# Kernel optimization log

Hardware: AMD Instinct MI355X
Metric: run time of the kernel (lower is better)

The kernel has to match this reference:

```python
import jax, jax.numpy as jnp
import numpy as np

BS, N, HD = 16, 96, 128      # batch, nodes per graph, hidden_nf
NL, NS = 4, 2                # n_layers, inv_sublayers
ND, HF = 3, 6                # n_dims, node feature dims (in_node_nf - time)
FIN = HF + 1                 # +1 time channel (condition_time=True)
NF = 100.0                   # normalization_factor, aggregation='sum'


def setup_inputs() -> dict:
    key = jax.random.key(0)
    ks = iter(jax.random.split(key, 40))

    def w(shape, scale=None):
        s = scale if scale is not None else 1.0 / np.sqrt(shape[-2])
        return jax.random.normal(next(ks), shape, jnp.float32) * s

    xh = jax.random.normal(next(ks), (BS, N, ND + HF), jnp.float32)
    t = jnp.array([0.5], jnp.float32)
    nm = (jax.random.uniform(next(ks), (BS, N, 1)) < 0.9).astype(jnp.float32)
    em = nm[:, :, None, :] * nm[:, None, :, :]
    em = em * (1.0 - jnp.eye(N, dtype=jnp.float32)[None, :, :, None])
    G = NL * NS
    return dict(
        xh=xh, t=t, node_mask=nm, edge_mask=em,
        W_emb=w((FIN, HD)), b_emb=jnp.zeros((HD,), jnp.float32),
        gWe1=w((G, 2 * HD + 2, HD)), gbe1=jnp.zeros((G, HD), jnp.float32),
        gWe2=w((G, HD, HD)), gbe2=jnp.zeros((G, HD), jnp.float32),
        gWn1=w((G, 2 * HD, HD)), gbn1=jnp.zeros((G, HD), jnp.float32),
        gWn2=w((G, HD, HD)), gbn2=jnp.zeros((G, HD), jnp.float32),
        eWc1=w((NL, 2 * HD + 2, HD)), ebc1=jnp.zeros((NL, HD), jnp.float32),
        eWc2=w((NL, HD, HD)), ebc2=jnp.zeros((NL, HD), jnp.float32),
        eWc3=w((NL, HD, 1), scale=0.001),   # xavier gain 0.001 as in EDM
        W_out=w((HD, FIN)), b_out=jnp.zeros((FIN,), jnp.float32),
    )


def _pair_mlp(h, ea, W1, b1, W2, b2):
    # silu(Linear(cat([h_i, h_j, ea]))) -> silu(Linear) without materializing the concat
    hi = h @ W1[:HD]            # (B,N,H) source part
    hj = h @ W1[HD:2 * HD]      # (B,N,H) target part
    m = jax.nn.silu(hi[:, :, None, :] + hj[:, None, :, :] + ea @ W1[2 * HD:] + b1)
    return jax.nn.silu(m @ W2 + b2)          # (B,N,N,H)


def _egnn(xh, t, node_mask, edge_mask, W_emb, b_emb, gWe1, gbe1, gWe2, gbe2,
          gWn1, gbn1, gWn2, gbn2, eWc1, ebc1, eWc2, ebc2, eWc3, W_out, b_out):
    xh = xh * node_mask                       # mask padded nodes
    x0 = xh[..., :ND]                         # (B,N,3)
    h_time = jnp.broadcast_to(t.reshape(1, 1, 1), (xh.shape[0], xh.shape[1], 1))
    h = jnp.concatenate([xh[..., ND:], h_time], axis=-1)   # (B,N,FIN)
    h = h @ W_emb + b_emb                     # node embedding
    # initial squared distances (EGNN-level edge_attr, in_edge_nf=1)
    d0 = jnp.sum((x0[:, :, None] - x0[:, None, :]) ** 2, -1, keepdims=True)
    x = x0
    for l in range(NL):                       # EquivariantBlocks
        diff = x[:, :, None] - x[:, None, :]  # x_i - x_j, (B,N,N,3)
        radial = jnp.sum(diff ** 2, -1, keepdims=True)
        coord_diff = diff / jnp.sqrt(radial + 1e-8)   # norm_constant=0
        ea = jnp.concatenate([radial, d0], axis=-1)   # (B,N,N,2)
        for s in range(NS):                   # GCL sublayers
            g = l * NS + s
            m = _pair_mlp(h, ea, gWe1[g], gbe1[g], gWe2[g], gbe2[g]) * edge_mask
            agg = jnp.sum(m, axis=2) / NF     # masked scatter-sum over j onto i
            u = jax.nn.silu(h @ gWn1[g, :HD] + agg @ gWn1[g, HD:] + gbn1[g])
            h = (h + (u @ gWn2[g] + gbn2[g])) * node_mask
        # EquivariantUpdate (tanh=False)
        phi = _pair_mlp(h, ea, eWc1[l], ebc1[l], eWc2[l], ebc2[l])
        trans = coord_diff * (phi @ eWc3[l]) * edge_mask    # (B,N,N,3)
        x = (x + jnp.sum(trans, axis=2) / NF) * node_mask
    h = (h @ W_out + b_out) * node_mask       # embedding_out
    vel = (x - x0) * node_mask
    # remove_mean_with_mask
    n_per = jnp.sum(node_mask, axis=1, keepdims=True)
    vel = vel - (jnp.sum(vel, axis=1, keepdims=True) / n_per) * node_mask
    # drop the appended time channel from h (condition_time=True, context=None)
    return jnp.concatenate([vel, h[..., :HF]], axis=-1)    # (B,N,3+HF)


def reference(xh, t, node_mask, edge_mask, W_emb, b_emb, gWe1, gbe1, gWe2, gbe2,
              gWn1, gbn1, gWn2, gbn2, eWc1, ebc1, eWc2, ebc2, eWc3, W_out, b_out):
    return _egnn(xh, t, node_mask, edge_mask, W_emb, b_emb, gWe1, gbe1, gWe2, gbe2,
                 gWn1, gbn1, gWn2, gbn2, eWc1, ebc1, eWc2, ebc2, eWc3, W_out, b_out)
```

## Files before the change

### kernel.cpp

```cpp
#include <hip/hip_runtime.h>
#include <hip/hip_bf16.h>

#define BSZ 16
#define Nn 96
#define HD 128
#define NDIM 3
#define HFEAT 6
#define FINC 7
#define BN (BSZ*Nn)

typedef const float* fp;
typedef __bf16 bf16x8_t __attribute__((ext_vector_type(8)));
typedef float  f32x4_t  __attribute__((ext_vector_type(4)));

__device__ __forceinline__ float silu(float x){ return x / (1.f + __expf(-x)); }
__device__ __forceinline__ unsigned short f2b(float x){
  unsigned u = __float_as_uint(x);
  unsigned r = u + 0x7FFF + ((u>>16)&1);
  return (unsigned short)(r>>16);
}
__device__ __forceinline__ unsigned pkf(float a, float b){
  __hip_bfloat162 h2 = __float22bfloat162_rn(make_float2(a,b));
  return *reinterpret_cast<unsigned*>(&h2);
}


__global__ void k_prep(fp gWe1, fp eWc1, fp gWe2, fp eWc2, fp gWn1, fp gWn2,
                       unsigned short* w1b, unsigned short* w2b,
                       unsigned short* wn1b, unsigned short* wn2b){
  int mid = blockIdx.x;
  if (mid < 12){
    const float* src = (mid<8)? gWe1 + (size_t)mid*258*HD : eWc1 + (size_t)(mid-8)*258*HD;
    unsigned short* dst = w1b + (size_t)mid*32768;
    for (int idx = threadIdx.x; idx < 32768; idx += 256){
      int jj = idx&7, l=(idx>>3)&63, kt=(idx>>9)&3, nt=idx>>11;
      int k = kt*32 + (l>>4)*8 + jj, n = nt*16 + (l&15);
      dst[idx] = f2b(src[(size_t)(k + ((n>>7)<<7))*HD + (n&127)]);
    }
  } else if (mid < 24){
    int m2 = mid-12;
    const float* src = (m2<8)? gWe2 + (size_t)m2*HD*HD : eWc2 + (size_t)(m2-8)*HD*HD;
    unsigned short* dst = w2b + (size_t)m2*HD*HD;
    for (int idx = threadIdx.x; idx < HD*HD; idx += 256){
      int jj = idx&7, l=(idx>>3)&63, kt=(idx>>9)&3, nt=idx>>11;
      int k = kt*32 + (l>>4)*8 + jj, n = nt*16 + (l&15);
      dst[idx] = f2b(src[k*HD+n]);
    }
  } else if (mid < 32){
    int g = mid-24;
    const float* src = gWn1 + (size_t)g*256*HD;
    unsigned short* dst = wn1b + (size_t)g*32768;
    for (int idx = threadIdx.x; idx < 32768; idx += 256){
      int jj = idx&7, l=(idx>>3)&63, kt=(idx>>9)&7, nt=idx>>12;
      int k = kt*32 + (l>>4)*8 + jj, n = nt*16 + (l&15);
      dst[idx] = f2b(src[(size_t)k*HD+n]);
    }
  } else {
    int g = mid-32;
    const float* src = gWn2 + (size_t)g*HD*HD;
    unsigned short* dst = wn2b + (size_t)g*HD*HD;
    for (int idx = threadIdx.x; idx < HD*HD; idx += 256){
      int jj = idx&7, l=(idx>>3)&63, kt=(idx>>9)&3, nt=idx>>11;
      int k = kt*32 + (l>>4)*8 + jj, n = nt*16 + (l&15);
      dst[idx] = f2b(src[k*HD+n]);
    }
  }
}

__global__ void k_embed(fp xh, fp t, fp nm, fp W_emb, fp b_emb,
                        float* h, float* x0, float* xA){
  int bn = blockIdx.x, tid = threadIdx.x;
  float nmv = nm[bn];
  if (tid < NDIM){
    float v = xh[bn*(NDIM+HFEAT)+tid] * nmv;
    x0[bn*3+tid] = v; xA[bn*3+tid] = v;
  }
  float acc = b_emb[tid];
  #pragma unroll
  for (int f=0; f<HFEAT; ++f)
    acc += xh[bn*(NDIM+HFEAT)+NDIM+f] * nmv * W_emb[f*HD+tid];
  acc += t[0] * W_emb[HFEAT*HD+tid];
  h[bn*HD+tid] = acc;
}

__global__ __launch_bounds__(256) void k_hij(const float* hin, const unsigned short* w1m,
                                             fp b1, float* Hi, float* Hj){
  __shared__ unsigned int hf[4*256];
  int tid=threadIdx.x, blk=blockIdx.x;
  int b = blk/6, mt = blk%6;
  int l=tid&63, w=tid>>6;
  { int kp=l, jsub=w;
    int kt=kp>>4, q=(kp>>2)&3, dsub=kp&3;
    int sm = kt + 4*(q&1);
    float2 hv[4];
    #pragma unroll
    for(int r=0;r<4;++r)
      hv[r] = ((const float2*)&hin[(size_t)(b*Nn+mt*16+jsub*4+r)*HD])[kp];
    #pragma unroll
    for(int r=0;r<4;++r){
      int row=jsub*4+r;
      hf[kt*256 + (((row + 16*q) ^ sm)<<2) + dsub] = pkf(hv[r].x,hv[r].y);
    } }
  __syncthreads();
  f32x4_t acc[4];
  #pragma unroll
  for(int s=0;s<4;++s) acc[s]=(f32x4_t){0.f,0.f,0.f,0.f};
  #pragma unroll
  for(int kt=0;kt<4;++kt){
    int pl = l ^ (kt + 4*((l>>4)&1));
    bf16x8_t A = *(const bf16x8_t*)((const unsigned int*)hf + kt*256 + pl*4);
    #pragma unroll
    for(int s=0;s<4;++s){
      bf16x8_t B = *(const bf16x8_t*)(w1m + ((((w*4+s)*4+kt)*64 + l)*8));
      acc[s]=__builtin_amdgcn_mfma_f32_16x16x32_bf16(A, B, acc[s], 0,0,0);
    }
  }
  #pragma unroll
  for(int s=0;s<4;++s){
    int nt=w*4+s, n=nt*16+(l&15);
    float b1v = (nt<8)? b1[n] : 0.f;
    #pragma unroll
    for(int r=0;r<4;++r){
      int R = b*Nn + mt*16 + (l>>4)*4 + r;
      float v = acc[s][r];
      if(nt<8) Hi[(size_t)R*HD+n] = v + b1v;
      else     Hj[(size_t)R*HD+(n-128)] = v;
    }
  }
}

__global__ __launch_bounds__(256,4) void k_pair(const float* Hi, const float* Hj,
    const float* x, const float* x0, fp nm, fp W1f,
    const unsigned short* w2m, fp b2, float* agg){
  __shared__ unsigned int m1f[24*256];
  __shared__ float xs[Nn][3], x0s[Nn][3], nms[Nn], rs[Nn], d0s[Nn];
  __shared__ float red[2][HD];
  int tid=threadIdx.x, bn=blockIdx.x;
  int b=bn/Nn, i=bn%Nn;
  int l=tid&63, w=tid>>6, wm=w>>1, wn=w&1;
  int jg=w;

  for(int idx=tid; idx<Nn*3; idx+=256){ int n=idx/3,d=idx%3;
    xs[n][d]=x[(b*Nn+n)*3+d]; x0s[n][d]=x0[(b*Nn+n)*3+d]; }
  if(tid<Nn) nms[tid]=nm[b*Nn+tid];
  __syncthreads();
  if(tid<Nn){
    float dx0=xs[i][0]-xs[tid][0], dx1=xs[i][1]-xs[tid][1], dx2=xs[i][2]-xs[tid][2];
    rs[tid]=dx0*dx0+dx1*dx1+dx2*dx2;
    float e0=x0s[i][0]-x0s[tid][0], e1=x0s[i][1]-x0s[tid][1], e2=x0s[i][2]-x0s[tid][2];
    d0s[tid]=e0*e0+e1*e1+e2*e2;
  }
  __syncthreads();

  { int kp=l;
    int kt2=kp>>4, q=(kp>>2)&3, dsub=kp&3;
    int sm=kt2+4*(q&1);
    float2 hi=((const float2*)&Hi[(size_t)bn*HD])[kp];
    float2 wr=((const float2*)&W1f[(size_t)(2*HD)*HD])[kp];
    float2 wd=((const float2*)&W1f[(size_t)(2*HD+1)*HD])[kp];
    const float2* HjB=(const float2*)&Hj[(size_t)(b*Nn)*HD];
    #pragma unroll
    for(int half=0; half<2; ++half){
      float2 hjv[12];
      #pragma unroll
      for(int u=0;u<12;++u){
        int rr=half*2+(u/6), mt2=u%6;
        int j=mt2*16+jg*4+rr;
        hjv[u]=HjB[(size_t)j*64+kp];
      }
      #pragma unroll
      for(int u=0;u<12;++u){
        int rr=half*2+(u/6), mt2=u%6;
        int jr=jg*4+rr, j=mt2*16+jr;
        float rv=rs[j], dv=d0s[j];
        float m0 =silu(hi.x+hjv[u].x+rv*wr.x+dv*wd.x);
        float m1v=silu(hi.y+hjv[u].y+rv*wr.y+dv*wd.y);
        m1f[mt2*1024 + kt2*256 + (((jr+16*q)^sm)<<2) + dsub]=pkf(m0,m1v);
      }
    } }
  __syncthreads();

  f32x4_t acc[3][4];
  #pragma unroll
  for(int a=0;a<3;++a)
    #pragma unroll
    for(int s=0;s<4;++s) acc[a][s]=(f32x4_t){0.f,0.f,0.f,0.f};
  #pragma unroll
  for(int kt=0;kt<4;++kt){
    int pl = l ^ (kt + 4*((l>>4)&1));
    bf16x8_t Bk[4];
    #pragma unroll
    for(int s=0;s<4;++s)
      Bk[s] = *(const bf16x8_t*)(w2m + ((((wn*4+s)*4+kt)*64 + l)*8));
    #pragma unroll
    for(int a=0;a<3;++a){
      bf16x8_t A = *(const bf16x8_t*)((const unsigned int*)m1f + (((wm*3+a)*4+kt)*256 + pl*4));
      #pragma unroll
      for(int s=0;s<4;++s)
        acc[a][s]=__builtin_amdgcn_mfma_f32_16x16x32_bf16(A, Bk[s], acc[a][s], 0,0,0);
    }
  }

  float b2v[4], p[4]={0.f,0.f,0.f,0.f};
  #pragma unroll
  for(int s=0;s<4;++s) b2v[s]=b2[(wn*4+s)*16 + (l&15)];
  #pragma unroll
  for(int a=0;a<3;++a)
    #pragma unroll
    for(int r=0;r<4;++r){
      int j=(wm*3+a)*16 + (l>>4)*4 + r;
      float emj=(j==i)?0.f:nms[j];
      #pragma unroll
      for(int s=0;s<4;++s) p[s] += silu(acc[a][s][r]+b2v[s])*emj;
    }
  #pragma unroll
  for(int s=0;s<4;++s){ p[s]+=__shfl_xor(p[s],16); p[s]+=__shfl_xor(p[s],32); }
  if(l<16){
    #pragma unroll
    for(int s=0;s<4;++s) red[wm][wn*64 + s*16 + l]=p[s];
  }
  __syncthreads();
  if(tid<HD) agg[(size_t)bn*HD+tid]=(red[0][tid]+red[1][tid])*nms[i]*(1.f/100.f);
}

__global__ __launch_bounds__(256) void k_nodehij(
    const float* hin, float* hout, const float* agg, fp nm,
    const unsigned short* wn1m, fp bn1v, const unsigned short* wn2m, fp bn2v,
    const unsigned short* w1mA, fp b1A, float* HiA, float* HjA,
    const unsigned short* w1mB, fp b1B, float* HiB, float* HjB){
  __shared__ unsigned int af[8*256];
  __shared__ float fbuf[16*132];
  __shared__ float nmr[16];
  int tid=threadIdx.x, blk=blockIdx.x;
  int b=blk/6, mt=blk%6;
  int R0=b*Nn+mt*16;
  int l=tid&63, w=tid>>6;
  int kp=l, jsub=w;
  int kt0=kp>>4, q=(kp>>2)&3, dsub=kp&3;
  int sm=kt0+4*(q&1);
  if(tid<16) nmr[tid]=nm[R0+tid];
  { float2 hv[4], av[4];
    #pragma unroll
    for(int r=0;r<4;++r){
      hv[r]=((const float2*)&hin[(size_t)(R0+jsub*4+r)*HD])[kp];
      av[r]=((const float2*)&agg[(size_t)(R0+jsub*4+r)*HD])[kp];
    }
    #pragma unroll
    for(int r=0;r<4;++r){
      int row=jsub*4+r;
      unsigned off=(((row+16*q)^sm)<<2)+dsub;
      af[kt0*256+off]=pkf(hv[r].x,hv[r].y);
      af[(4+kt0)*256+off]=pkf(av[r].x,av[r].y);
    } }
  __syncthreads();
  f32x4_t c1[2];
  c1[0]=(f32x4_t){0.f,0.f,0.f,0.f}; c1[1]=(f32x4_t){0.f,0.f,0.f,0.f};
  #pragma unroll
  for(int t=0;t<8;++t){
    int pl = l ^ ((t&3) + 4*((l>>4)&1));
    bf16x8_t A=*(const bf16x8_t*)((const unsigned int*)af + t*256 + pl*4);
    #pragma unroll
    for(int s=0;s<2;++s){
      bf16x8_t B=*(const bf16x8_t*)(wn1m + ((((2*w+s)*8+t)*64+l)*8));
      c1[s]=__builtin_amdgcn_mfma_f32_16x16x32_bf16(A,B,c1[s],0,0,0);
    }
  }
  #pragma unroll
  for(int s=0;s<2;++s){
    int n=(2*w+s)*16+(l&15);
    float bv=bn1v[n];
    #pragma unroll
    for(int r=0;r<4;++r){
      int row=(l>>4)*4+r;
      fbuf[row*132+n]=silu(c1[s][r]+bv);
    }
  }
  __syncthreads();
  #pragma unroll
  for(int r=0;r<4;++r){
    int row=jsub*4+r;
    float2 uv=*(const float2*)&fbuf[row*132+2*kp];
    af[kt0*256 + (((row+16*q)^sm)<<2)+dsub]=pkf(uv.x,uv.y);
  }
  __syncthreads();
  f32x4_t c2[2];
  c2[0]=(f32x4_t){0.f,0.f,0.f,0.f}; c2[1]=(f32x4_t){0.f,0.f,0.f,0.f};
  #pragma unroll
  for(int t=0;t<4;++t){
    int pl = l ^ (t + 4*((l>>4)&1));
    bf16x8_t A=*(const bf16x8_t*)((const unsigned int*)af + t*256 + pl*4);
    #pragma unroll
    for(int s=0;s<2;++s){
      bf16x8_t B=*(const bf16x8_t*)(wn2m + ((((2*w+s)*4+t)*64+l)*8));
      c2[s]=__builtin_amdgcn_mfma_f32_16x16x32_bf16(A,B,c2[s],0,0,0);
    }
  }
  { float hv[2][4];
    #pragma unroll
    for(int s=0;s<2;++s){
      int n=(2*w+s)*16+(l&15);
      #pragma unroll
      for(int r=0;r<4;++r)
        hv[s][r]=hin[(size_t)(R0+(l>>4)*4+r)*HD+n];
    }
    #pragma unroll
    for(int s=0;s<2;++s){
      int n=(2*w+s)*16+(l&15);
      float bv=bn2v[n];
      #pragma unroll
      for(int r=0;r<4;++r){
        int row=(l>>4)*4+r;
        float val=(hv[s][r]+c2[s][r]+bv)*nmr[row];
        hout[(size_t)(R0+row)*HD+n]=val;
        fbuf[row*132+n]=val;
      }
    } }
  __syncthreads();
  #pragma unroll
  for(int r=0;r<4;++r){
    int row=jsub*4+r;
    float2 uv=*(const float2*)&fbuf[row*132+2*kp];
    af[kt0*256 + (((row+16*q)^sm)<<2)+dsub]=pkf(uv.x,uv.y);
  }
  __syncthreads();
  {
    f32x4_t a3[4];
    #pragma unroll
    for(int s=0;s<4;++s) a3[s]=(f32x4_t){0.f,0.f,0.f,0.f};
    #pragma unroll
    for(int t=0;t<4;++t){
      int pl = l ^ (t + 4*((l>>4)&1));
      bf16x8_t A=*(const bf16x8_t*)((const unsigned int*)af + t*256 + pl*4);
      #pragma unroll
      for(int s=0;s<4;++s){
        bf16x8_t B=*(const bf16x8_t*)(w1mA + ((((w*4+s)*4+t)*64+l)*8));
        a3[s]=__builtin_amdgcn_mfma_f32_16x16x32_bf16(A,B,a3[s],0,0,0);
      }
    }
    #pragma unroll
    for(int s=0;s<4;++s){
      int nt=w*4+s, n=nt*16+(l&15);
      float b1v=(nt<8)? b1A[n] : 0.f;
      #pragma unroll
      for(int r=0;r<4;++r){
        int R=R0+(l>>4)*4+r;
        float v=a3[s][r];
        if(nt<8) HiA[(size_t)R*HD+n]=v+b1v;
        else     HjA[(size_t)R*HD+(n-128)]=v;
      }
    }
  }
  if(w1mB){
    f32x4_t a3[4];
    #pragma unroll
    for(int s=0;s<4;++s) a3[s]=(f32x4_t){0.f,0.f,0.f,0.f};
    #pragma unroll
    for(int t=0;t<4;++t){
      int pl = l ^ (t + 4*((l>>4)&1));
      bf16x8_t A=*(const bf16x8_t*)((const unsigned int*)af + t*256 + pl*4);
      #pragma unroll
      for(int s=0;s<4;++s){
        bf16x8_t B=*(const bf16x8_t*)(w1mB + ((((w*4+s)*4+t)*64+l)*8));
        a3[s]=__builtin_amdgcn_mfma_f32_16x16x32_bf16(A,B,a3[s],0,0,0);
      }
    }
    #pragma unroll
    for(int s=0;s<4;++s){
      int nt=w*4+s, n=nt*16+(l&15);
      float b1v=(nt<8)? b1B[n] : 0.f;
      #pragma unroll
      for(int r=0;r<4;++r){
        int R=R0+(l>>4)*4+r;
        float v=a3[s][r];
        if(nt<8) HiB[(size_t)R*HD+n]=v+b1v;
        else     HjB[(size_t)R*HD+(n-128)]=v;
      }
    }
  }
}

__global__ __launch_bounds__(256,4) void k_coord(const float* Hi, const float* Hj,
    const float* x, const float* x0, fp nm, fp W1f,
    const unsigned short* w2m, fp b2, fp W3, float* xn){
  __shared__ unsigned int m1f[24*256];
  __shared__ float xs[Nn][3], x0s[Nn][3], nms[Nn], rs[Nn], d0s[Nn];
  __shared__ float redJ[2][Nn];
  __shared__ float sjs[Nn];
  int tid=threadIdx.x, bn=blockIdx.x;
  int b=bn/Nn, i=bn%Nn;
  int l=tid&63, w=tid>>6, wm=w>>1, wn=w&1;
  int jg=w;

  for(int idx=tid; idx<Nn*3; idx+=256){ int n=idx/3,d=idx%3;
    xs[n][d]=x[(b*Nn+n)*3+d]; x0s[n][d]=x0[(b*Nn+n)*3+d]; }
  if(tid<Nn) nms[tid]=nm[b*Nn+tid];
  __syncthreads();
  if(tid<Nn){
    float dx0=xs[i][0]-xs[tid][0], dx1=xs[i][1]-xs[tid][1], dx2=xs[i][2]-xs[tid][2];
    rs[tid]=dx0*dx0+dx1*dx1+dx2*dx2;
    float e0=x0s[i][0]-x0s[tid][0], e1=x0s[i][1]-x0s[tid][1], e2=x0s[i][2]-x0s[tid][2];
    d0s[tid]=e0*e0+e1*e1+e2*e2;
  }
  __syncthreads();

  { int kp=l;
    int kt2=kp>>4, q=(kp>>2)&3, dsub=kp&3;
    int sm=kt2+4*(q&1);
    float2 hi=((const float2*)&Hi[(size_t)bn*HD])[kp];
    float2 wr=((const float2*)&W1f[(size_t)(2*HD)*HD])[kp];
    float2 wd=((const float2*)&W1f[(size_t)(2*HD+1)*HD])[kp];
    const float2* HjB=(const float2*)&Hj[(size_t)(b*Nn)*HD];
    #pragma unroll
    for(int half=0; half<2; ++half){
      float2 hjv[12];
      #pragma unroll
      for(int u=0;u<12;++u){
        int rr=half*2+(u/6), mt2=u%6;
        int j=mt2*16+jg*4+rr;
        hjv[u]=HjB[(size_t)j*64+kp];
      }
      #pragma unroll
      for(int u=0;u<12;++u){
        int rr=half*2+(u/6), mt2=u%6;
        int jr=jg*4+rr, j=mt2*16+jr;
        float rv=rs[j], dv=d0s[j];
        float m0 =silu(hi.x+hjv[u].x+rv*wr.x+dv*wd.x);
        float m1v=silu(hi.y+hjv[u].y+rv*wr.y+dv*wd.y);
        m1f[mt2*1024 + kt2*256 + (((jr+16*q)^sm)<<2) + dsub]=pkf(m0,m1v);
      }
    } }
  __syncthreads();

  f32x4_t acc[3][4];
  #pragma unroll
  for(int a=0;a<3;++a)
    #pragma unroll
    for(int s=0;s<4;++s) acc[a][s]=(f32x4_t){0.f,0.f,0.f,0.f};
  #pragma unroll
  for(int kt=0;kt<4;++kt){
    int pl = l ^ (kt + 4*((l>>4)&1));
    bf16x8_t Bk[4];
    #pragma unroll
    for(int s=0;s<4;++s)
      Bk[s] = *(const bf16x8_t*)(w2m + ((((wn*4+s)*4+kt)*64 + l)*8));
    #pragma unroll
    for(int a=0;a<3;++a){
      bf16x8_t A = *(const bf16x8_t*)((const unsigned int*)m1f + (((wm*3+a)*4+kt)*256 + pl*4));
      #pragma unroll
      for(int s=0;s<4;++s)
        acc[a][s]=__builtin_amdgcn_mfma_f32_16x16x32_bf16(A, Bk[s], acc[a][s], 0,0,0);
    }
  }

  float b2v[4], w3v[4];
  #pragma unroll
  for(int s=0;s<4;++s){ b2v[s]=b2[(wn*4+s)*16+(l&15)]; w3v[s]=W3[(wn*4+s)*16+(l&15)]; }
  float qv[3][4];
  #pragma unroll
  for(int a=0;a<3;++a)
    #pragma unroll
    for(int r=0;r<4;++r){
      float pj=0.f;
      #pragma unroll
      for(int s=0;s<4;++s) pj += silu(acc[a][s][r]+b2v[s])*w3v[s];
      qv[a][r]=pj;
    }
  #pragma unroll
  for(int d=1;d<16;d<<=1)
    #pragma unroll
    for(int a=0;a<3;++a)
      #pragma unroll
      for(int r=0;r<4;++r)
        qv[a][r] += __shfl_xor(qv[a][r], d);
  if((l&15)==0){
    int quad=l>>4;
    #pragma unroll
    for(int a=0;a<3;++a)
      #pragma unroll
      for(int r=0;r<4;++r)
        redJ[wn][(wm*3+a)*16 + quad*4 + r]=qv[a][r];
  }
  __syncthreads();
  if(tid<Nn){
    float pj=redJ[0][tid]+redJ[1][tid];
    float em=(tid==i)?0.f:nms[tid];
    sjs[tid]=pj*em*rsqrtf(rs[tid]+1e-8f);
  }
  __syncthreads();
  if(w<3){
    int d=w;
    float xi=xs[i][d];
    float s=(xi-xs[l][d])*sjs[l];
    if(l<32) s += (xi-xs[l+64][d])*sjs[l+64];
    s+=__shfl_xor(s,1); s+=__shfl_xor(s,2); s+=__shfl_xor(s,4);
    s+=__shfl_xor(s,8); s+=__shfl_xor(s,16); s+=__shfl_xor(s,32);
    if(l==0) xn[(size_t)(b*Nn+i)*3+d]=(xi+s*(1.f/100.f))*nms[i];
  }
}

__global__ void k_velstat(const float* xf, const float* x0, fp nm, float* vstat){
  __shared__ float sh[128];
  int b=blockIdx.x, tid=threadIdx.x;
  float nmv = (tid<Nn)? nm[b*Nn+tid] : 0.f;
  float vals[4];
  #pragma unroll
  for(int d=0;d<3;++d)
    vals[d] = (tid<Nn)? (xf[(b*Nn+tid)*3+d]-x0[(b*Nn+tid)*3+d])*nmv : 0.f;
  vals[3]=nmv;
  #pragma unroll
  for(int q=0;q<4;++q){
    sh[tid]=vals[q]; __syncthreads();
    for(int s=64;s>0;s>>=1){ if(tid<s) sh[tid]+=sh[tid+s]; __syncthreads(); }
    if(tid==0) vstat[b*4+q]=sh[0];
    __syncthreads();
  }
}

__global__ void k_out(const float* h, const float* xf, const float* x0, fp nm,
                      const float* vstat, fp W_out, fp b_out, float* out){
  __shared__ float shh[HD];
  int bn=blockIdx.x, tid=threadIdx.x, b=bn/Nn;
  shh[tid]=h[bn*HD+tid]; __syncthreads();
  float nmv=nm[bn];
  if(tid<3){
    float vel=(xf[bn*3+tid]-x0[bn*3+tid])*nmv;
    float mean=vstat[b*4+tid]/vstat[b*4+3];
    out[bn*(NDIM+HFEAT)+tid]=vel-mean*nmv;
  } else if(tid<3+HFEAT){
    int f=tid-3;
    float acc=b_out[f];
    for(int k=0;k<HD;++k) acc+=shh[k]*W_out[k*FINC+f];
    out[bn*(NDIM+HFEAT)+tid]=acc*nmv;
  }
}

extern "C" void kernel_launch(void* const* d_in, const int* in_sizes, int n_in,
                              void* d_out, int out_size, void* d_ws, size_t ws_size,
                              hipStream_t stream) {
  fp xh   =(fp)d_in[0];
  fp t    =(fp)d_in[1];
  fp nm   =(fp)d_in[2];
  fp W_emb=(fp)d_in[4],  b_emb=(fp)d_in[5];
  fp gWe1 =(fp)d_in[6],  gbe1 =(fp)d_in[7];
  fp gWe2 =(fp)d_in[8],  gbe2 =(fp)d_in[9];
  fp gWn1 =(fp)d_in[10], gbn1 =(fp)d_in[11];
  fp gWn2 =(fp)d_in[12], gbn2 =(fp)d_in[13];
  fp eWc1 =(fp)d_in[14], ebc1 =(fp)d_in[15];
  fp eWc2 =(fp)d_in[16], ebc2 =(fp)d_in[17];
  fp eWc3 =(fp)d_in[18];
  fp W_out=(fp)d_in[19], b_out=(fp)d_in[20];

  unsigned short* w1b  = (unsigned short*)d_ws;
  unsigned short* w2b  = w1b  + (size_t)12*32768;
  unsigned short* wn1b = w2b  + (size_t)12*16384;
  unsigned short* wn2b = wn1b + (size_t)8*32768;
  float* fbase = (float*)(wn2b + (size_t)8*16384);
  float* hA   = fbase;
  float* hB   = hA  + BN*HD;
  float* HiA  = hB  + BN*HD;
  float* HjA  = HiA + BN*HD;
  float* HiE  = HjA + BN*HD;
  float* HjE  = HiE + BN*HD;
  float* agg  = HjE + BN*HD;
  float* x0   = agg + BN*HD;
  float* xA   = x0  + BN*3;
  float* xB   = xA  + BN*3;
  float* vstat= xB  + BN*3;

  k_prep <<<40,256,0,stream>>>(gWe1, eWc1, gWe2, eWc2, gWn1, gWn2, w1b, w2b, wn1b, wn2b);
  k_embed<<<BN,128,0,stream>>>(xh,t,nm,W_emb,b_emb,hA,x0,xA);
  k_hij  <<<96,256,0,stream>>>(hA, w1b, gbe1, HiA, HjA);
  float *hc=hA, *hn=hB, *xc=xA, *xn=xB;
  for(int l=0;l<4;++l){
    int g=2*l;
    k_pair<<<BN,256,0,stream>>>(HiA,HjA,xc,x0,nm, gWe1+(size_t)g*258*HD,
          w2b+(size_t)g*HD*HD, gbe2+(size_t)g*HD, agg);
    k_nodehij<<<96,256,0,stream>>>(hc,hn,agg,nm,
          wn1b+(size_t)g*32768, gbn1+(size_t)g*HD,
          wn2b+(size_t)g*16384, gbn2+(size_t)g*HD,
          w1b+(size_t)(g+1)*32768, gbe1+(size_t)(g+1)*HD, HiA, HjA,
          nullptr, nullptr, nullptr, nullptr);
    { float* tmp=hc; hc=hn; hn=tmp; }
    g=2*l+1;
    k_pair<<<BN,256,0,stream>>>(HiA,HjA,xc,x0,nm, gWe1+(size_t)g*258*HD,
          w2b+(size_t)g*HD*HD, gbe2+(size_t)g*HD, agg);
    bool last = (l==3);
    k_nodehij<<<96,256,0,stream>>>(hc,hn,agg,nm,
          wn1b+(size_t)g*32768, gbn1+(size_t)g*HD,
          wn2b+(size_t)g*16384, gbn2+(size_t)g*HD,
          w1b+(size_t)(8+l)*32768, ebc1+(size_t)l*HD, HiE, HjE,
          last? nullptr : w1b+(size_t)(g+1)*32768,
          last? nullptr : gbe1+(size_t)(g+1)*HD, HiA, HjA);
    { float* tmp=hc; hc=hn; hn=tmp; }
    k_coord<<<BN,256,0,stream>>>(HiE,HjE,xc,x0,nm, eWc1+(size_t)l*258*HD,
          w2b+(size_t)(8+l)*HD*HD, ebc2+(size_t)l*HD,
          eWc3+(size_t)l*HD, xn);
    { float* tmp=xc; xc=xn; xn=tmp; }
  }
  k_velstat<<<BSZ,128,0,stream>>>(xc,x0,nm,vstat);
  k_out   <<<BN,128,0,stream>>>(hc,xc,x0,nm,vstat,W_out,b_out,(float*)d_out);
}
```

Measured before the change: 527.3 us.

## Process two source nodes per block in pair and coord kernels

k_pair and k_coord now handle two i nodes per block instead of one, halving the grid. The Hj row loads, weight B-fragment loads and setup work are shared across both nodes, which is meant to cut global/L2 traffic and per-block overhead. The cost is double the LDS per block and a launch-bounds occupancy hint lowered from 4 to 3, which reduces concurrent blocks and may limit latency hiding.

```diff
diff --git a/kernel.cpp b/kernel.cpp
--- a/kernel.cpp
+++ b/kernel.cpp
@@ -129,33 +129,33 @@
   }
 }
 
-__global__ __launch_bounds__(256,4) void k_pair(const float* Hi, const float* Hj,
+__global__ __launch_bounds__(256,3) void k_pair(const float* Hi, const float* Hj,
     const float* x, const float* x0, fp nm, fp W1f,
     const unsigned short* w2m, fp b2, float* agg){
-  __shared__ unsigned int m1f[24*256];
-  __shared__ float xs[Nn][3], x0s[Nn][3], nms[Nn], rs[Nn], d0s[Nn];
-  __shared__ float red[2][HD];
-  int tid=threadIdx.x, bn=blockIdx.x;
-  int b=bn/Nn, i=bn%Nn;
+  __shared__ unsigned int m1f[2][24*256];
+  __shared__ float nms[Nn], rs[2][Nn], d0s[2][Nn];
+  int tid=threadIdx.x, blk=blockIdx.x;
+  int b=blk/48, i0=(blk%48)*2;
   int l=tid&63, w=tid>>6, wm=w>>1, wn=w&1;
   int jg=w;
 
-  for(int idx=tid; idx<Nn*3; idx+=256){ int n=idx/3,d=idx%3;
-    xs[n][d]=x[(b*Nn+n)*3+d]; x0s[n][d]=x0[(b*Nn+n)*3+d]; }
   if(tid<Nn) nms[tid]=nm[b*Nn+tid];
-  __syncthreads();
-  if(tid<Nn){
-    float dx0=xs[i][0]-xs[tid][0], dx1=xs[i][1]-xs[tid][1], dx2=xs[i][2]-xs[tid][2];
-    rs[tid]=dx0*dx0+dx1*dx1+dx2*dx2;
-    float e0=x0s[i][0]-x0s[tid][0], e1=x0s[i][1]-x0s[tid][1], e2=x0s[i][2]-x0s[tid][2];
-    d0s[tid]=e0*e0+e1*e1+e2*e2;
+  if((tid&127)<Nn){
+    int ii=tid>>7, j=tid&127, i=i0+ii;
+    const float* xb=&x[(size_t)(b*Nn)*3];
+    const float* x0b=&x0[(size_t)(b*Nn)*3];
+    float dx0=xb[i*3]-xb[j*3], dx1=xb[i*3+1]-xb[j*3+1], dx2=xb[i*3+2]-xb[j*3+2];
+    rs[ii][j]=dx0*dx0+dx1*dx1+dx2*dx2;
+    float e0=x0b[i*3]-x0b[j*3], e1=x0b[i*3+1]-x0b[j*3+1], e2=x0b[i*3+2]-x0b[j*3+2];
+    d0s[ii][j]=e0*e0+e1*e1+e2*e2;
   }
   __syncthreads();
 
   { int kp=l;
-    int kt2=kp>>4, q=(kp>>2)&3, dsub=kp&3;
-    int sm=kt2+4*(q&1);
-    float2 hi=((const float2*)&Hi[(size_t)bn*HD])[kp];
+    int kt2=kp>>4, qd=(kp>>2)&3, dsub=kp&3;
+    int sm=kt2+4*(qd&1);
+    float2 hi0=((const float2*)&Hi[(size_t)(b*Nn+i0)*HD])[kp];
+    float2 hi1=((const float2*)&Hi[(size_t)(b*Nn+i0+1)*HD])[kp];
     float2 wr=((const float2*)&W1f[(size_t)(2*HD)*HD])[kp];
     float2 wd=((const float2*)&W1f[(size_t)(2*HD+1)*HD])[kp];
     const float2* HjB=(const float2*)&Hj[(size_t)(b*Nn)*HD];
@@ -172,55 +172,69 @@
       for(int u=0;u<12;++u){
         int rr=half*2+(u/6), mt2=u%6;
         int jr=jg*4+rr, j=mt2*16+jr;
-        float rv=rs[j], dv=d0s[j];
-        float m0 =silu(hi.x+hjv[u].x+rv*wr.x+dv*wd.x);
-        float m1v=silu(hi.y+hjv[u].y+rv*wr.y+dv*wd.y);
-        m1f[mt2*1024 + kt2*256 + (((jr+16*q)^sm)<<2) + dsub]=pkf(m0,m1v);
+        unsigned addr = mt2*1024 + kt2*256 + (((jr+16*qd)^sm)<<2) + dsub;
+        float r0=rs[0][j], dd0=d0s[0][j];
+        float r1=rs[1][j], dd1=d0s[1][j];
+        m1f[0][addr]=pkf(silu(hi0.x+hjv[u].x+r0*wr.x+dd0*wd.x),
+                         silu(hi0.y+hjv[u].y+r0*wr.y+dd0*wd.y));
+        m1f[1][addr]=pkf(silu(hi1.x+hjv[u].x+r1*wr.x+dd1*wd.x),
+                         silu(hi1.y+hjv[u].y+r1*wr.y+dd1*wd.y));
       }
     } }
   __syncthreads();
 
-  f32x4_t acc[3][4];
-  #pragma unroll
-  for(int a=0;a<3;++a)
-    #pragma unroll
-    for(int s=0;s<4;++s) acc[a][s]=(f32x4_t){0.f,0.f,0.f,0.f};
-  #pragma unroll
-  for(int kt=0;kt<4;++kt){
-    int pl = l ^ (kt + 4*((l>>4)&1));
-    bf16x8_t Bk[4];
-    #pragma unroll
-    for(int s=0;s<4;++s)
-      Bk[s] = *(const bf16x8_t*)(w2m + ((((wn*4+s)*4+kt)*64 + l)*8));
-    #pragma unroll
-    for(int a=0;a<3;++a){
-      bf16x8_t A = *(const bf16x8_t*)((const unsigned int*)m1f + (((wm*3+a)*4+kt)*256 + pl*4));
+  float b2v[4];
+  #pragma unroll
+  for(int s=0;s<4;++s) b2v[s]=b2[(wn*4+s)*16 + (l&15)];
+  float pv[2][4];
+  #pragma unroll
+  for(int ii=0; ii<2; ++ii){
+    f32x4_t acc[3][4];
+    #pragma unroll
+    for(int a=0;a<3;++a)
+      #pragma unroll
+      for(int s=0;s<4;++s) acc[a][s]=(f32x4_t){0.f,0.f,0.f,0.f};
+    #pragma unroll
+    for(int kt=0;kt<4;++kt){
+      int pl = l ^ (kt + 4*((l>>4)&1));
+      bf16x8_t Bk[4];
       #pragma unroll
       for(int s=0;s<4;++s)
-        acc[a][s]=__builtin_amdgcn_mfma_f32_16x16x32_bf16(A, Bk[s], acc[a][s], 0,0,0);
-    }
-  }
-
-  float b2v[4], p[4]={0.f,0.f,0.f,0.f};
-  #pragma unroll
-  for(int s=0;s<4;++s) b2v[s]=b2[(wn*4+s)*16 + (l&15)];
-  #pragma unroll
-  for(int a=0;a<3;++a)
-    #pragma unroll
-    for(int r=0;r<4;++r){
-      int j=(wm*3+a)*16 + (l>>4)*4 + r;
-      float emj=(j==i)?0.f:nms[j];
-      #pragma unroll
-      for(int s=0;s<4;++s) p[s] += silu(acc[a][s][r]+b2v[s])*emj;
-    }
-  #pragma unroll
-  for(int s=0;s<4;++s){ p[s]+=__shfl_xor(p[s],16); p[s]+=__shfl_xor(p[s],32); }
+        Bk[s] = *(const bf16x8_t*)(w2m + ((((wn*4+s)*4+kt)*64 + l)*8));
+      #pragma unroll
+      for(int a=0;a<3;++a){
+        bf16x8_t A = *(const bf16x8_t*)((const unsigned int*)m1f[ii] + (((wm*3+a)*4+kt)*256 + pl*4));
+        #pragma unroll
+        for(int s=0;s<4;++s)
+          acc[a][s]=__builtin_amdgcn_mfma_f32_16x16x32_bf16(A, Bk[s], acc[a][s], 0,0,0);
+      }
+    }
+    float p[4]={0.f,0.f,0.f,0.f};
+    int i=i0+ii;
+    #pragma unroll
+    for(int a=0;a<3;++a)
+      #pragma unroll
+      for(int r=0;r<4;++r){
+        int j=(wm*3+a)*16 + (l>>4)*4 + r;
+        float emj=(j==i)?0.f:nms[j];
+        #pragma unroll
+        for(int s=0;s<4;++s) p[s] += silu(acc[a][s][r]+b2v[s])*emj;
+      }
+    #pragma unroll
+    for(int s=0;s<4;++s){ p[s]+=__shfl_xor(p[s],16); p[s]+=__shfl_xor(p[s],32); pv[ii][s]=p[s]; }
+  }
+  __syncthreads();
+  float* redf=(float*)m1f;
   if(l<16){
     #pragma unroll
-    for(int s=0;s<4;++s) red[wm][wn*64 + s*16 + l]=p[s];
-  }
-  __syncthreads();
-  if(tid<HD) agg[(size_t)bn*HD+tid]=(red[0][tid]+red[1][tid])*nms[i]*(1.f/100.f);
+    for(int ii=0;ii<2;++ii)
+      #pragma unroll
+      for(int s=0;s<4;++s) redf[(wm*2+ii)*128 + wn*64 + s*16 + l]=pv[ii][s];
+  }
+  __syncthreads();
+  { int ii=tid>>7, c=tid&127;
+    agg[(size_t)(b*Nn+i0+ii)*HD+c]=(redf[ii*128+c]+redf[(2+ii)*128+c])*nms[i0+ii]*(1.f/100.f);
+  }
 }
 
 __global__ __launch_bounds__(256) void k_nodehij(
@@ -379,34 +393,35 @@
   }
 }
 
-__global__ __launch_bounds__(256,4) void k_coord(const float* Hi, const float* Hj,
+__global__ __launch_bounds__(256,3) void k_coord(const float* Hi, const float* Hj,
     const float* x, const float* x0, fp nm, fp W1f,
     const unsigned short* w2m, fp b2, fp W3, float* xn){
-  __shared__ unsigned int m1f[24*256];
-  __shared__ float xs[Nn][3], x0s[Nn][3], nms[Nn], rs[Nn], d0s[Nn];
-  __shared__ float redJ[2][Nn];
-  __shared__ float sjs[Nn];
-  int tid=threadIdx.x, bn=blockIdx.x;
-  int b=bn/Nn, i=bn%Nn;
+  __shared__ unsigned int m1f[2][24*256];
+  __shared__ float xs[Nn][3], nms[Nn], rs[2][Nn], d0s[2][Nn], sjs[2][Nn];
+  int tid=threadIdx.x, blk=blockIdx.x;
+  int b=blk/48, i0=(blk%48)*2;
   int l=tid&63, w=tid>>6, wm=w>>1, wn=w&1;
   int jg=w;
 
   for(int idx=tid; idx<Nn*3; idx+=256){ int n=idx/3,d=idx%3;
-    xs[n][d]=x[(b*Nn+n)*3+d]; x0s[n][d]=x0[(b*Nn+n)*3+d]; }
+    xs[n][d]=x[(b*Nn+n)*3+d]; }
   if(tid<Nn) nms[tid]=nm[b*Nn+tid];
-  __syncthreads();
-  if(tid<Nn){
-    float dx0=xs[i][0]-xs[tid][0], dx1=xs[i][1]-xs[tid][1], dx2=xs[i][2]-xs[tid][2];
-    rs[tid]=dx0*dx0+dx1*dx1+dx2*dx2;
-    float e0=x0s[i][0]-x0s[tid][0], e1=x0s[i][1]-x0s[tid][1], e2=x0s[i][2]-x0s[tid][2];
-    d0s[tid]=e0*e0+e1*e1+e2*e2;
+  if((tid&127)<Nn){
+    int ii=tid>>7, j=tid&127, i=i0+ii;
+    const float* xb=&x[(size_t)(b*Nn)*3];
+    const float* x0b=&x0[(size_t)(b*Nn)*3];
+    float dx0=xb[i*3]-xb[j*3], dx1=xb[i*3+1]-xb[j*3+1], dx2=xb[i*3+2]-xb[j*3+2];
+    rs[ii][j]=dx0*dx0+dx1*dx1+dx2*dx2;
+    float e0=x0b[i*3]-x0b[j*3], e1=x0b[i*3+1]-x0b[j*3+1], e2=x0b[i*3+2]-x0b[j*3+2];
+    d0s[ii][j]=e0*e0+e1*e1+e2*e2;
   }
   __syncthreads();
 
   { int kp=l;
-    int kt2=kp>>4, q=(kp>>2)&3, dsub=kp&3;
-    int sm=kt2+4*(q&1);
-    float2 hi=((const float2*)&Hi[(size_t)bn*HD])[kp];
+    int kt2=kp>>4, qd=(kp>>2)&3, dsub=kp&3;
+    int sm=kt2+4*(qd&1);
+    float2 hi0=((const float2*)&Hi[(size_t)(b*Nn+i0)*HD])[kp];
+    float2 hi1=((const float2*)&Hi[(size_t)(b*Nn+i0+1)*HD])[kp];
     float2 wr=((const float2*)&W1f[(size_t)(2*HD)*HD])[kp];
     float2 wd=((const float2*)&W1f[(size_t)(2*HD+1)*HD])[kp];
     const float2* HjB=(const float2*)&Hj[(size_t)(b*Nn)*HD];
@@ -423,78 +438,92 @@
       for(int u=0;u<12;++u){
         int rr=half*2+(u/6), mt2=u%6;
         int jr=jg*4+rr, j=mt2*16+jr;
-        float rv=rs[j], dv=d0s[j];
-        float m0 =silu(hi.x+hjv[u].x+rv*wr.x+dv*wd.x);
-        float m1v=silu(hi.y+hjv[u].y+rv*wr.y+dv*wd.y);
-        m1f[mt2*1024 + kt2*256 + (((jr+16*q)^sm)<<2) + dsub]=pkf(m0,m1v);
+        unsigned addr = mt2*1024 + kt2*256 + (((jr+16*qd)^sm)<<2) + dsub;
+        float r0=rs[0][j], dd0=d0s[0][j];
+        float r1=rs[1][j], dd1=d0s[1][j];
+        m1f[0][addr]=pkf(silu(hi0.x+hjv[u].x+r0*wr.x+dd0*wd.x),
+                         silu(hi0.y+hjv[u].y+r0*wr.y+dd0*wd.y));
+        m1f[1][addr]=pkf(silu(hi1.x+hjv[u].x+r1*wr.x+dd1*wd.x),
+                         silu(hi1.y+hjv[u].y+r1*wr.y+dd1*wd.y));
       }
     } }
   __syncthreads();
 
-  f32x4_t acc[3][4];
-  #pragma unroll
-  for(int a=0;a<3;++a)
-    #pragma unroll
-    for(int s=0;s<4;++s) acc[a][s]=(f32x4_t){0.f,0.f,0.f,0.f};
-  #pragma unroll
-  for(int kt=0;kt<4;++kt){
-    int pl = l ^ (kt + 4*((l>>4)&1));
-    bf16x8_t Bk[4];
-    #pragma unroll
-    for(int s=0;s<4;++s)
-      Bk[s] = *(const bf16x8_t*)(w2m + ((((wn*4+s)*4+kt)*64 + l)*8));
-    #pragma unroll
-    for(int a=0;a<3;++a){
-      bf16x8_t A = *(const bf16x8_t*)((const unsigned int*)m1f + (((wm*3+a)*4+kt)*256 + pl*4));
+  float b2v[4], w3v[4];
+  #pragma unroll
+  for(int s=0;s<4;++s){ b2v[s]=b2[(wn*4+s)*16+(l&15)]; w3v[s]=W3[(wn*4+s)*16+(l&15)]; }
+  float qvv[2][3][4];
+  #pragma unroll
+  for(int ii=0; ii<2; ++ii){
+    f32x4_t acc[3][4];
+    #pragma unroll
+    for(int a=0;a<3;++a)
+      #pragma unroll
+      for(int s=0;s<4;++s) acc[a][s]=(f32x4_t){0.f,0.f,0.f,0.f};
+    #pragma unroll
+    for(int kt=0;kt<4;++kt){
+      int pl = l ^ (kt + 4*((l>>4)&1));
+      bf16x8_t Bk[4];
       #pragma unroll
       for(int s=0;s<4;++s)
-        acc[a][s]=__builtin_amdgcn_mfma_f32_16x16x32_bf16(A, Bk[s], acc[a][s], 0,0,0);
-    }
-  }
-
-  float b2v[4], w3v[4];
-  #pragma unroll
-  for(int s=0;s<4;++s){ b2v[s]=b2[(wn*4+s)*16+(l&15)]; w3v[s]=W3[(wn*4+s)*16+(l&15)]; }
-  float qv[3][4];
-  #pragma unroll
-  for(int a=0;a<3;++a)
-    #pragma unroll
-    for(int r=0;r<4;++r){
-      float pj=0.f;
-      #pragma unroll
-      for(int s=0;s<4;++s) pj += silu(acc[a][s][r]+b2v[s])*w3v[s];
-      qv[a][r]=pj;
-    }
-  #pragma unroll
-  for(int d=1;d<16;d<<=1)
+        Bk[s] = *(const bf16x8_t*)(w2m + ((((wn*4+s)*4+kt)*64 + l)*8));
+      #pragma unroll
+      for(int a=0;a<3;++a){
+        bf16x8_t A = *(const bf16x8_t*)((const unsigned int*)m1f[ii] + (((wm*3+a)*4+kt)*256 + pl*4));
+        #pragma unroll
+        for(int s=0;s<4;++s)
+          acc[a][s]=__builtin_amdgcn_mfma_f32_16x16x32_bf16(A, Bk[s], acc[a][s], 0,0,0);
+      }
+    }
     #pragma unroll
     for(int a=0;a<3;++a)
       #pragma unroll
-      for(int r=0;r<4;++r)
-        qv[a][r] += __shfl_xor(qv[a][r], d);
+      for(int r=0;r<4;++r){
+        float pj=0.f;
+        #pragma unroll
+        for(int s=0;s<4;++s) pj += silu(acc[a][s][r]+b2v[s])*w3v[s];
+        qvv[ii][a][r]=pj;
+      }
+    #pragma unroll
+    for(int d=1;d<16;d<<=1)
+      #pragma unroll
+      for(int a=0;a<3;++a)
+        #pragma unroll
+        for(int r=0;r<4;++r)
+          qvv[ii][a][r] += __shfl_xor(qvv[ii][a][r], d);
+  }
+  __syncthreads();
+  float* redjf=(float*)m1f;
   if((l&15)==0){
     int quad=l>>4;
     #pragma unroll
-    for(int a=0;a<3;++a)
-      #pragma unroll
-      for(int r=0;r<4;++r)
-        redJ[wn][(wm*3+a)*16 + quad*4 + r]=qv[a][r];
-  }
-  __syncthreads();
-  if(tid<Nn){
-    float pj=redJ[0][tid]+redJ[1][tid];
-    float em=(tid==i)?0.f:nms[tid];
-    sjs[tid]=pj*em*rsqrtf(rs[tid]+1e-8f);
+    for(int ii=0;ii<2;++ii)
+      #pragma unroll
+      for(int a=0;a<3;++a)
+        #pragma unroll
+        for(int r=0;r<4;++r)
+          redjf[(wn*2+ii)*Nn + (wm*3+a)*16 + quad*4 + r]=qvv[ii][a][r];
+  }
+  __syncthreads();
+  if((tid&127)<Nn){
+    int ii=tid>>7, j=tid&127, i=i0+ii;
+    float pj=redjf[ii*Nn+j]+redjf[(2+ii)*Nn+j];
+    float em=(j==i)?0.f:nms[j];
+    sjs[ii][j]=pj*em*rsqrtf(rs[ii][j]+1e-8f);
   }
   __syncthreads();
   if(w<3){
     int d=w;
-    float xi=xs[i][d];
-    float s=(xi-xs[l][d])*sjs[l];
-    if(l<32) s += (xi-xs[l+64][d])*sjs[l+64];
-    s+=__shfl_xor(s,1); s+=__shfl_xor(s,2); s+=__shfl_xor(s,4);
-    s+=__shfl_xor(s,8); s+=__shfl_xor(s,16); s+=__shfl_xor(s,32);
-    if(l==0) xn[(size_t)(b*Nn+i)*3+d]=(xi+s*(1.f/100.f))*nms[i];
+    #pragma unroll
+    for(int ii=0;ii<2;++ii){
+      int i=i0+ii;
+      float xi=xs[i][d];
+      float s=(xi-xs[l][d])*sjs[ii][l];
+      if(l<32) s += (xi-xs[l+64][d])*sjs[ii][l+64];
+      s+=__shfl_xor(s,1); s+=__shfl_xor(s,2); s+=__shfl_xor(s,4);
+      s+=__shfl_xor(s,8); s+=__shfl_xor(s,16); s+=__shfl_xor(s,32);
+      if(l==0) xn[(size_t)(b*Nn+i)*3+d]=(xi+s*(1.f/100.f))*nms[i];
+    }
   }
 }
 
@@ -573,7 +602,7 @@
   float *hc=hA, *hn=hB, *xc=xA, *xn=xB;
   for(int l=0;l<4;++l){
     int g=2*l;
-    k_pair<<<BN,256,0,stream>>>(HiA,HjA,xc,x0,nm, gWe1+(size_t)g*258*HD,
+    k_pair<<<BN/2,256,0,stream>>>(HiA,HjA,xc,x0,nm, gWe1+(size_t)g*258*HD,
           w2b+(size_t)g*HD*HD, gbe2+(size_t)g*HD, agg);
     k_nodehij<<<96,256,0,stream>>>(hc,hn,agg,nm,
           wn1b+(size_t)g*32768, gbn1+(size_t)g*HD,
@@ -582,7 +611,7 @@
           nullptr, nullptr, nullptr, nullptr);
     { float* tmp=hc; hc=hn; hn=tmp; }
     g=2*l+1;
-    k_pair<<<BN,256,0,stream>>>(HiA,HjA,xc,x0,nm, gWe1+(size_t)g*258*HD,
+    k_pair<<<BN/2,256,0,stream>>>(HiA,HjA,xc,x0,nm, gWe1+(size_t)g*258*HD,
           w2b+(size_t)g*HD*HD, gbe2+(size_t)g*HD, agg);
     bool last = (l==3);
     k_nodehij<<<96,256,0,stream>>>(hc,hn,agg,nm,
@@ -592,7 +621,7 @@
           last? nullptr : w1b+(size_t)(g+1)*32768,
           last? nullptr : gbe1+(size_t)(g+1)*HD, HiA, HjA);
     { float* tmp=hc; hc=hn; hn=tmp; }
-    k_coord<<<BN,256,0,stream>>>(HiE,HjE,xc,x0,nm, eWc1+(size_t)l*258*HD,
+    k_coord<<<BN/2,256,0,stream>>>(HiE,HjE,xc,x0,nm, eWc1+(size_t)l*258*HD,
           w2b+(size_t)(8+l)*HD*HD, ebc2+(size_t)l*HD,
           eWc3+(size_t)l*HD, xn);
     { float* tmp=xc; xc=xn; xn=tmp; }
```

After: 535.0 us. Within noise of the previous version (+1.5%).
